# Kernel optimization log

Measured on AMD Instinct MI355X. Metric: run time of the kernel, lower is better.

Reference implementation:

```python
import jax, jax.numpy as jnp
import numpy as np

H = 256          # decoder_size
V = 3            # vocab_size
MAX_LENGTH = 64


def lstm_cell(x, h, c, Wih, Whh, b):
    # PyTorch gate order: i, f, g, o
    g = x @ Wih.T + h @ Whh.T + b
    i, f, gg, o = jnp.split(g, 4, axis=-1)
    c = jax.nn.sigmoid(f) * c + jax.nn.sigmoid(i) * jnp.tanh(gg)
    h = jax.nn.sigmoid(o) * jnp.tanh(c)
    return h, c


def setup_inputs() -> dict:
    key = jax.random.key(0)
    ks = jax.random.split(key, 16)
    T, B, F = 512, 32, 1024
    s = 1.0 / np.sqrt(H)
    u = lambda k, shape: jax.random.uniform(k, shape, jnp.float32, -s, s)
    return dict(
        cnn_feats=jax.random.normal(ks[0], (T, B, F), jnp.float32),
        # bidirectional encoder LSTM (1 layer)
        enc_Wih_f=u(ks[1], (4 * H, F)), enc_Whh_f=u(ks[2], (4 * H, H)), enc_b_f=u(ks[3], (4 * H,)),
        enc_Wih_b=u(ks[4], (4 * H, F)), enc_Whh_b=u(ks[5], (4 * H, H)), enc_b_b=u(ks[6], (4 * H,)),
        # 2-layer decoder LSTM
        dec_Wih0=u(ks[7], (4 * H, H)), dec_Whh0=u(ks[8], (4 * H, H)), dec_b0=u(ks[9], (4 * H,)),
        dec_Wih1=u(ks[10], (4 * H, H)), dec_Whh1=u(ks[11], (4 * H, H)), dec_b1=u(ks[12], (4 * H,)),
        # per-step output projection
        lin_W=u(ks[13], (V, H)), lin_b=u(ks[14], (V,)),
    )


def _forward(cnn_feats, enc_Wih_f, enc_Whh_f, enc_b_f, enc_Wih_b, enc_Whh_b, enc_b_b,
             dec_Wih0, dec_Whh0, dec_b0, dec_Wih1, dec_Whh1, dec_b1, lin_W, lin_b):
    B = cnn_feats.shape[1]
    z = jnp.zeros((B, H), cnn_feats.dtype)

    def run_dir(seq, Wih, Whh, b):
        def step(carry, x):
            h, c = lstm_cell(x, carry[0], carry[1], Wih, Whh, b)
            return (h, c), None
        (h, c), _ = jax.lax.scan(step, (z, z), seq)
        return h, c

    # encoder final states: fwd over seq, bwd over reversed seq
    hf, cf = run_dir(cnn_feats, enc_Wih_f, enc_Whh_f, enc_b_f)
    hb, cb = run_dir(cnn_feats[::-1], enc_Wih_b, enc_Whh_b, enc_b_b)

    # decoder: layer0 init = fwd-dir state, layer1 init = bwd-dir state
    def dstep(carry, _):
        x, h0, c0, h1, c1 = carry
        h0, c0 = lstm_cell(x, h0, c0, dec_Wih0, dec_Whh0, dec_b0)
        h1, c1 = lstm_cell(h0, h1, c1, dec_Wih1, dec_Whh1, dec_b1)
        y = h1 @ lin_W.T + lin_b
        return (h1, h0, c0, h1, c1), y

    _, ys = jax.lax.scan(dstep, (z, hf, cf, hb, cb), None, length=MAX_LENGTH)
    return ys  # (MAX_LENGTH, B, V)


def reference(cnn_feats, enc_Wih_f, enc_Whh_f, enc_b_f, enc_Wih_b, enc_Whh_b, enc_b_b,
              dec_Wih0, dec_Whh0, dec_b0, dec_Wih1, dec_Whh1, dec_b1, lin_W, lin_b):
    return _forward(cnn_feats, enc_Wih_f, enc_Whh_f, enc_b_f, enc_Wih_b, enc_Whh_b, enc_b_b,
                    dec_Wih0, dec_Whh0, dec_b0, dec_Wih1, dec_Whh1, dec_b1, lin_W, lin_b)
```

## Files before the change

### kernel.cpp

```cpp
#include <hip/hip_runtime.h>
#include <stdint.h>
#include <stddef.h>

typedef __attribute__((ext_vector_type(8))) short  short8;
typedef __attribute__((ext_vector_type(4))) float  floatx4;
typedef unsigned long long u64;

#define SENT 0xAAAAAAAAAAAAAAAAull

static __device__ __forceinline__ float b2f(uint16_t h) {
  union { uint32_t u; float f; } v; v.u = ((uint32_t)h) << 16; return v.f;
}
static __device__ __forceinline__ uint16_t f2b(float f) {
  union { float f; uint32_t u; } v; v.f = f;
  uint32_t u = v.u;
  uint32_t r = u + 0x7FFFu + ((u >> 16) & 1u);
  return (uint16_t)(r >> 16);
}
static __device__ __forceinline__ float sigm(float x)  { return 1.0f / (1.0f + __expf(-x)); }
static __device__ __forceinline__ float tanh_f(float x){ return 1.0f - 2.0f / (1.0f + __expf(2.0f * x)); }

static __device__ __forceinline__ floatx4 mfma16(short8 a, short8 b, floatx4 c) {
  return __builtin_amdgcn_mfma_f32_16x16x32_bf16(a, b, c, 0, 0, 0);
}
static __device__ __forceinline__ short8 cvt8(const float* p) {
  short8 r;
  #pragma unroll
  for (int i = 0; i < 8; ++i) r[i] = (short)f2b(p[i]);
  return r;
}
static __device__ __forceinline__ u64 ld_h64(const u64* p) {
  return __hip_atomic_load(p, __ATOMIC_RELAXED, __HIP_MEMORY_SCOPE_AGENT);
}
static __device__ __forceinline__ void st_h64(uint16_t* p, u64 v) {
  __hip_atomic_store((u64*)p, v, __ATOMIC_RELAXED, __HIP_MEMORY_SCOPE_AGENT);
}
static __device__ __forceinline__ void poll8(const u64* p, u64* o) {
  for (;;) {
    bool ok = true;
    #pragma unroll
    for (int i = 0; i < 8; ++i) { o[i] = ld_h64(p + i); ok &= (o[i] != SENT); }
    if (ok) break;
    __builtin_amdgcn_s_sleep(1);
  }
}

#define H 256
#define FH 1024
#define BATCH 32
#define TSEQ 512
#define DSTEPS 64
#define ERING 8

__global__ __launch_bounds__(256) void gemm_xw(
    const float* __restrict__ A, const float* __restrict__ W,
    const float* __restrict__ bias, void* __restrict__ Cout, int out_f32)
{
  const int K = 1024, N = 1024;
  __shared__ uint16_t Ah[64 * 40], Al[64 * 40];
  __shared__ uint16_t Wh[64 * 40], Wl[64 * 40];
  const int m0 = blockIdx.x * 64;
  const int n0 = blockIdx.y * 64;
  const int tid = threadIdx.x;
  const int lane = tid & 63, w = tid >> 6;
  const int wm = w & 1, wn = w >> 1;
  const int l15 = lane & 15, q4 = lane >> 4;
  const int ldrow = tid >> 2, ldk = (tid & 3) * 8;

  floatx4 acc[2][2];
  for (int i = 0; i < 2; ++i) for (int j = 0; j < 2; ++j) acc[i][j] = (floatx4){0.f,0.f,0.f,0.f};

  for (int kb = 0; kb < K; kb += 32) {
    float aa[8], ww[8];
    {
      const float4* ap = (const float4*)(A + (size_t)(m0 + ldrow) * K + kb + ldk);
      const float4* wp = (const float4*)(W + (size_t)(n0 + ldrow) * K + kb + ldk);
      *(float4*)(aa) = ap[0]; *(float4*)(aa + 4) = ap[1];
      *(float4*)(ww) = wp[0]; *(float4*)(ww + 4) = wp[1];
    }
    short8 ah, al, wh, wl;
    #pragma unroll
    for (int i = 0; i < 8; ++i) {
      uint16_t h = f2b(aa[i]); ah[i] = (short)h; al[i] = (short)f2b(aa[i] - b2f(h));
      uint16_t g = f2b(ww[i]); wl[i] = (short)f2b(ww[i] - b2f(f2b(ww[i]) ? 0 : 0));
      wh[i] = (short)f2b(ww[i]); wl[i] = (short)f2b(ww[i] - b2f((uint16_t)wh[i]));
    }
    __syncthreads();
    *(short8*)(Ah + ldrow * 40 + ldk) = ah;
    *(short8*)(Al + ldrow * 40 + ldk) = al;
    *(short8*)(Wh + ldrow * 40 + ldk) = wh;
    *(short8*)(Wl + ldrow * 40 + ldk) = wl;
    __syncthreads();
    short8 afh[2], afl[2], bfh[2], bfl[2];
    #pragma unroll
    for (int mt = 0; mt < 2; ++mt) {
      afh[mt] = *(const short8*)(Ah + (wm * 32 + mt * 16 + l15) * 40 + q4 * 8);
      afl[mt] = *(const short8*)(Al + (wm * 32 + mt * 16 + l15) * 40 + q4 * 8);
    }
    #pragma unroll
    for (int nt = 0; nt < 2; ++nt) {
      bfh[nt] = *(const short8*)(Wh + (wn * 32 + nt * 16 + l15) * 40 + q4 * 8);
      bfl[nt] = *(const short8*)(Wl + (wn * 32 + nt * 16 + l15) * 40 + q4 * 8);
    }
    #pragma unroll
    for (int mt = 0; mt < 2; ++mt)
      #pragma unroll
      for (int nt = 0; nt < 2; ++nt) {
        acc[mt][nt] = mfma16(afh[mt], bfh[nt], acc[mt][nt]);
        acc[mt][nt] = mfma16(afh[mt], bfl[nt], acc[mt][nt]);
        acc[mt][nt] = mfma16(afl[mt], bfh[nt], acc[mt][nt]);
      }
  }
  #pragma unroll
  for (int mt = 0; mt < 2; ++mt)
    #pragma unroll
    for (int nt = 0; nt < 2; ++nt) {
      const int col = n0 + wn * 32 + nt * 16 + l15;
      const float bv = bias[col];
      #pragma unroll
      for (int r = 0; r < 4; ++r) {
        const int row = m0 + wm * 32 + mt * 16 + q4 * 4 + r;
        const float v = acc[mt][nt][r] + bv;
        if (out_f32) ((float*)Cout)[(size_t)row * N + col] = v;
        else         ((uint16_t*)Cout)[(size_t)row * N + col] = f2b(v);
      }
    }
}

__global__ __launch_bounds__(256, 1) void enc_rnn(
    const void* __restrict__ XgF, const void* __restrict__ XgB, int xg_f32,
    const float* __restrict__ WhhF, const float* __restrict__ WhhB,
    uint16_t* __restrict__ hslots,
    uint16_t* __restrict__ hfin, float* __restrict__ cfin)
{
  const int d = blockIdx.x >> 3, q = blockIdx.x & 7;
  const void*  Xg  = d ? XgB : XgF;
  const float* Whh = d ? WhhB : WhhF;
  uint16_t* hsl = hslots + d * (ERING * BATCH * H);
  const int jOff = q * 32;
  const int tid = threadIdx.x, lane = tid & 63, w = tid >> 6;
  const int tt = w & 1, nt = w >> 1, l15 = lane & 15, q4 = lane >> 4;
  const int b = nt * 16 + l15;
  const int jg = jOff + tt * 16 + q4 * 4;

  __shared__ uint16_t hS[2][32 * 264];
  __shared__ float    xgS[2][32 * 132];

  short8 Af[4][8];
  #pragma unroll
  for (int g = 0; g < 4; ++g) {
    const int grow = g * H + jOff + tt * 16 + l15;
    #pragma unroll
    for (int ks = 0; ks < 8; ++ks)
      Af[g][ks] = cvt8(Whh + (size_t)grow * H + ks * 32 + q4 * 8);
  }
  for (int i = tid; i < 32 * 264; i += 256) hS[0][i] = 0;

  float cc[4] = {0.f, 0.f, 0.f, 0.f};
  union HV { uint16_t u16[4]; u64 v; } hv; hv.v = 0ull;
  const int rb = tid >> 3, seg = tid & 7;
  const int cp = seg * 16;
  const int gge = cp >> 5, jj = cp & 31;

  for (int s = 0; s < TSEQ; ++s) {
    const int t = d ? (TSEQ - 1 - s) : s;
    const int p = s & 1;
    float xv[16];
    {
      const size_t base = (size_t)(t * BATCH + rb) * FH + gge * H + jOff + jj;
      if (xg_f32) {
        const float4* xs = (const float4*)((const float*)Xg + base);
        *(float4*)(xv) = xs[0]; *(float4*)(xv + 4) = xs[1];
        *(float4*)(xv + 8) = xs[2]; *(float4*)(xv + 12) = xs[3];
      } else {
        const uint16_t* xs = (const uint16_t*)Xg + base;
        #pragma unroll
        for (int i = 0; i < 16; ++i) xv[i] = b2f(xs[i]);
      }
    }

    if (s > 0) {
      u64 tmp[8];
      const u64* ps = (const u64*)(hsl + ((s - 1) & (ERING - 1)) * (BATCH * H) + rb * H + seg * 32);
      poll8(ps, tmp);
      #pragma unroll
      for (int i = 0; i < 8; ++i)
        *(u64*)(hS[p] + rb * 264 + seg * 32 + i * 4) = tmp[i];
    }
    if (s >= 2)
      st_h64(hsl + ((s - 2) & (ERING - 1)) * (BATCH * H) + b * H + jg, SENT);
    #pragma unroll
    for (int i = 0; i < 16; ++i) xgS[p][rb * 132 + cp + i] = xv[i];
    __syncthreads();

    floatx4 a0 = {0.f,0.f,0.f,0.f}, a1 = a0, a2 = a0, a3 = a0;
    #pragma unroll
    for (int ks = 0; ks < 8; ++ks) {
      short8 bfv = *(const short8*)(hS[p] + b * 264 + ks * 32 + q4 * 8);
      a0 = mfma16(Af[0][ks], bfv, a0);
      a1 = mfma16(Af[1][ks], bfv, a1);
      a2 = mfma16(Af[2][ks], bfv, a2);
      a3 = mfma16(Af[3][ks], bfv, a3);
    }
    #pragma unroll
    for (int r = 0; r < 4; ++r) {
      const int jl = tt * 16 + q4 * 4 + r;
      const float gi = a0[r] + xgS[p][b * 132 +      jl];
      const float gf = a1[r] + xgS[p][b * 132 + 32 + jl];
      const float gc = a2[r] + xgS[p][b * 132 + 64 + jl];
      const float go = a3[r] + xgS[p][b * 132 + 96 + jl];
      const float cn2 = sigm(gf) * cc[r] + sigm(gi) * tanh_f(gc);
      cc[r] = cn2;
      hv.u16[r] = f2b(sigm(go) * tanh_f(cn2));
    }
    st_h64(hsl + (s & (ERING - 1)) * (BATCH * H) + b * H + jg, hv.v);
  }
  #pragma unroll
  for (int r = 0; r < 4; ++r) {
    hfin[d * (BATCH * H) + b * H + jg + r] = hv.u16[r];
    cfin[d * (BATCH * H) + b * H + jg + r] = cc[r];
  }
}

__global__ __launch_bounds__(256, 1) void dec_rnn(
    const float* __restrict__ Wih0, const float* __restrict__ Whh0, const float* __restrict__ bb0,
    const float* __restrict__ Wih1, const float* __restrict__ Whh1, const float* __restrict__ bb1,
    const uint16_t* __restrict__ hfin, const float* __restrict__ cfin,
    uint16_t* __restrict__ h0slots,
    uint16_t* __restrict__ h1slots,
    float*    __restrict__ h1f)
{
  const int L = blockIdx.x >> 3, q = blockIdx.x & 7;
  const float* Wih = L ? Wih1 : Wih0;
  const float* Whh = L ? Whh1 : Whh0;
  const float* bs  = L ? bb1 : bb0;
  const int jOff = q * 32;
  const int tid = threadIdx.x, lane = tid & 63, w = tid >> 6;
  const int tt = w & 1, nt = w >> 1, l15 = lane & 15, q4 = lane >> 4;
  const int b = nt * 16 + l15;
  const int jg = jOff + tt * 16 + q4 * 4;

  __shared__ uint16_t xhS[2][32 * 528];

  short8 Af[4][16];
  #pragma unroll
  for (int g = 0; g < 4; ++g) {
    const int grow = g * H + jOff + tt * 16 + l15;
    #pragma unroll
    for (int ks = 0; ks < 8; ++ks) {
      Af[g][ks]     = cvt8(Wih + (size_t)grow * H + ks * 32 + q4 * 8);
      Af[g][8 + ks] = cvt8(Whh + (size_t)grow * H + ks * 32 + q4 * 8);
    }
  }
  float brg[4][4];
  #pragma unroll
  for (int g = 0; g < 4; ++g)
    #pragma unroll
    for (int r = 0; r < 4; ++r)
      brg[g][r] = bs[g * H + jOff + tt * 16 + q4 * 4 + r];

  float cc[4];
  #pragma unroll
  for (int r = 0; r < 4; ++r) cc[r] = cfin[L * (BATCH * H) + b * H + jg + r];

  const int rb = tid >> 3, seg = tid & 7;
  const size_t off = (size_t)rb * H + seg * 32;
  union HV { uint16_t u16[4]; u64 v; } hv; hv.v = 0ull;

  for (int t = 0; t < DSTEPS; ++t) {
    const int p = t & 1;
    u64 tx[8], th[8];
    if (t == 0) {
      const u64* ph = (const u64*)(hfin + L * (BATCH * H) + off);
      #pragma unroll
      for (int i = 0; i < 8; ++i) th[i] = ph[i];
    } else {
      const uint16_t* hb = (L ? h1slots : h0slots) + (size_t)(t - 1) * (BATCH * H);
      poll8((const u64*)(hb + off), th);
    }
    if (L == 0) {
      if (t == 0) {
        #pragma unroll
        for (int i = 0; i < 8; ++i) tx[i] = 0ull;
      } else {
        poll8((const u64*)(h1slots + (size_t)(t - 1) * (BATCH * H) + off), tx);
      }
    } else {
      poll8((const u64*)(h0slots + (size_t)t * (BATCH * H) + off), tx);
    }
    #pragma unroll
    for (int i = 0; i < 8; ++i) {
      *(u64*)(xhS[p] + rb * 528 + seg * 32 + i * 4) = tx[i];
      *(u64*)(xhS[p] + rb * 528 + 256 + seg * 32 + i * 4) = th[i];
    }
    __syncthreads();

    floatx4 a0 = {0.f,0.f,0.f,0.f}, a1 = a0, a2 = a0, a3 = a0;
    #pragma unroll
    for (int ks = 0; ks < 16; ++ks) {
      short8 bfv = *(const short8*)(xhS[p] + b * 528 + ks * 32 + q4 * 8);
      a0 = mfma16(Af[0][ks], bfv, a0);
      a1 = mfma16(Af[1][ks], bfv, a1);
      a2 = mfma16(Af[2][ks], bfv, a2);
      a3 = mfma16(Af[3][ks], bfv, a3);
    }
    float hval[4];
    #pragma unroll
    for (int r = 0; r < 4; ++r) {
      const float gi = a0[r] + brg[0][r];
      const float gf = a1[r] + brg[1][r];
      const float gc = a2[r] + brg[2][r];
      const float go = a3[r] + brg[3][r];
      const float cn2 = sigm(gf) * cc[r] + sigm(gi) * tanh_f(gc);
      cc[r] = cn2;
      hval[r] = sigm(go) * tanh_f(cn2);
      hv.u16[r] = f2b(hval[r]);
    }
    st_h64((L ? h1slots : h0slots) + (size_t)t * (BATCH * H) + b * H + jg, hv.v);
    if (L == 1) {
      float* df = h1f + (size_t)t * (BATCH * H) + b * H + jg;
      #pragma unroll
      for (int r = 0; r < 4; ++r) df[r] = hval[r];
    }
  }
}

__global__ __launch_bounds__(256) void out_proj(
    const float* __restrict__ h1f, const float* __restrict__ linW,
    const float* __restrict__ linb, float* __restrict__ out)
{
  const int idx = blockIdx.x * 256 + threadIdx.x;
  if (idx >= DSTEPS * BATCH * 3) return;
  const int v = idx % 3;
  const int tb = idx / 3;
  const float* hrow = h1f + (size_t)tb * H;
  const float* wrow = linW + (size_t)v * H;
  float s = linb[v];
  for (int k = 0; k < H; ++k) s += hrow[k] * wrow[k];
  out[idx] = s;
}

extern "C" void kernel_launch(void* const* d_in, const int* in_sizes, int n_in,
                              void* d_out, int out_size, void* d_ws, size_t ws_size,
                              hipStream_t stream) {
  (void)in_sizes; (void)n_in; (void)out_size;
  const float* cnn   = (const float*)d_in[0];
  const float* WihF  = (const float*)d_in[1];
  const float* WhhF  = (const float*)d_in[2];
  const float* bF    = (const float*)d_in[3];
  const float* WihB  = (const float*)d_in[4];
  const float* WhhB  = (const float*)d_in[5];
  const float* bB    = (const float*)d_in[6];
  const float* Wih0  = (const float*)d_in[7];
  const float* Whh0  = (const float*)d_in[8];
  const float* b0    = (const float*)d_in[9];
  const float* Wih1  = (const float*)d_in[10];
  const float* Whh1  = (const float*)d_in[11];
  const float* b1    = (const float*)d_in[12];
  const float* linW  = (const float*)d_in[13];
  const float* linb  = (const float*)d_in[14];

  const size_t XG_ELEMS = (size_t)TSEQ * BATCH * FH;
  const size_t SMALL = 2457600;
  const int xg_f32 = (ws_size >= 2 * XG_ELEMS * 4 + SMALL) ? 1 : 0;
  const size_t S = XG_ELEMS * (xg_f32 ? 4 : 2);

  uint8_t* ws = (uint8_t*)d_ws;
  void*     XgF    = (void*)(ws);
  void*     XgB    = (void*)(ws + S);
  float*    h1f    = (float*)(ws + S);
  uint8_t*  base   = ws + 2 * S;
  uint16_t* hslotsE = (uint16_t*)(base);
  uint16_t* h0slots = (uint16_t*)(base + 262144);
  uint16_t* h1slots = (uint16_t*)(base + 1310720);
  uint16_t* hfin    = (uint16_t*)(base + 2359296);
  float*    cfin    = (float*)(base + 2392064);

  hipMemsetAsync(base, 0xAA, 2359296, stream);

  gemm_xw<<<dim3(256, 16), 256, 0, stream>>>(cnn, WihF, bF, XgF, xg_f32);
  gemm_xw<<<dim3(256, 16), 256, 0, stream>>>(cnn, WihB, bB, XgB, xg_f32);
  enc_rnn<<<16, 256, 0, stream>>>(XgF, XgB, xg_f32, WhhF, WhhB,
                                  hslotsE, hfin, cfin);
  dec_rnn<<<16, 256, 0, stream>>>(Wih0, Whh0, b0, Wih1, Whh1, b1,
                                  hfin, cfin, h0slots, h1slots, h1f);
  out_proj<<<24, 256, 0, stream>>>(h1f, linW, linb, (float*)d_out);
}
```

Baseline: 2.587 ms.

## Poll hidden-state fragments directly into MFMA registers, dropping LDS staging and barriers

The encoder and decoder recurrent kernels no longer stage polled hidden states and input gates through shared memory behind __syncthreads. Each lane now polls exactly the MFMA B-fragment it needs with cache-bypassing dwordx4 inline-asm loads and feeds it straight to the MFMAs. The encoder also prefetches the next step's input-gate values into registers and resets the ring slot from further back, which widens the slack before a slot is reused. Each lane now reads redundant global data, and correctness relies on slot-reset ordering across a deeper ring lag and a periodic atomic-load fallback in the poll loop.

```diff
diff --git a/kernel.cpp b/kernel.cpp
--- a/kernel.cpp
+++ b/kernel.cpp
@@ -4,6 +4,7 @@
 
 typedef __attribute__((ext_vector_type(8))) short  short8;
 typedef __attribute__((ext_vector_type(4))) float  floatx4;
+typedef __attribute__((ext_vector_type(4))) unsigned int u32x4;
 typedef unsigned long long u64;
 
 #define SENT 0xAAAAAAAAAAAAAAAAull
@@ -29,17 +30,90 @@
   for (int i = 0; i < 8; ++i) r[i] = (short)f2b(p[i]);
   return r;
 }
+
+static __device__ __forceinline__ void st_h64(uint16_t* p, u64 v) {
+  __hip_atomic_store((u64*)p, v, __ATOMIC_RELAXED, __HIP_MEMORY_SCOPE_AGENT);
+}
 static __device__ __forceinline__ u64 ld_h64(const u64* p) {
   return __hip_atomic_load(p, __ATOMIC_RELAXED, __HIP_MEMORY_SCOPE_AGENT);
 }
-static __device__ __forceinline__ void st_h64(uint16_t* p, u64 v) {
-  __hip_atomic_store((u64*)p, v, __ATOMIC_RELAXED, __HIP_MEMORY_SCOPE_AGENT);
-}
-static __device__ __forceinline__ void poll8(const u64* p, u64* o) {
+static __device__ __forceinline__ bool frag_ok(u32x4 v) {
+  const u64 lo = ((u64)v[1] << 32) | v[0];
+  const u64 hi = ((u64)v[3] << 32) | v[2];
+  return (lo != SENT) & (hi != SENT);
+}
+static __device__ __forceinline__ void ld8x16(const uint16_t* p, u32x4* o) {
+  asm volatile(
+      "global_load_dwordx4 %0, %8, off sc0 sc1\n\t"
+      "global_load_dwordx4 %1, %8, off offset:64 sc0 sc1\n\t"
+      "global_load_dwordx4 %2, %8, off offset:128 sc0 sc1\n\t"
+      "global_load_dwordx4 %3, %8, off offset:192 sc0 sc1\n\t"
+      "global_load_dwordx4 %4, %8, off offset:256 sc0 sc1\n\t"
+      "global_load_dwordx4 %5, %8, off offset:320 sc0 sc1\n\t"
+      "global_load_dwordx4 %6, %8, off offset:384 sc0 sc1\n\t"
+      "global_load_dwordx4 %7, %8, off offset:448 sc0 sc1\n\t"
+      "s_waitcnt vmcnt(0)"
+      : "=&v"(o[0]), "=&v"(o[1]), "=&v"(o[2]), "=&v"(o[3]),
+        "=&v"(o[4]), "=&v"(o[5]), "=&v"(o[6]), "=&v"(o[7])
+      : "v"(p)
+      : "memory");
+}
+static __device__ __forceinline__ void ld16x16(const uint16_t* pa, const uint16_t* pb,
+                                               u32x4* oa, u32x4* ob) {
+  asm volatile(
+      "global_load_dwordx4 %0, %16, off sc0 sc1\n\t"
+      "global_load_dwordx4 %1, %16, off offset:64 sc0 sc1\n\t"
+      "global_load_dwordx4 %2, %16, off offset:128 sc0 sc1\n\t"
+      "global_load_dwordx4 %3, %16, off offset:192 sc0 sc1\n\t"
+      "global_load_dwordx4 %4, %16, off offset:256 sc0 sc1\n\t"
+      "global_load_dwordx4 %5, %16, off offset:320 sc0 sc1\n\t"
+      "global_load_dwordx4 %6, %16, off offset:384 sc0 sc1\n\t"
+      "global_load_dwordx4 %7, %16, off offset:448 sc0 sc1\n\t"
+      "global_load_dwordx4 %8, %17, off sc0 sc1\n\t"
+      "global_load_dwordx4 %9, %17, off offset:64 sc0 sc1\n\t"
+      "global_load_dwordx4 %10, %17, off offset:128 sc0 sc1\n\t"
+      "global_load_dwordx4 %11, %17, off offset:192 sc0 sc1\n\t"
+      "global_load_dwordx4 %12, %17, off offset:256 sc0 sc1\n\t"
+      "global_load_dwordx4 %13, %17, off offset:320 sc0 sc1\n\t"
+      "global_load_dwordx4 %14, %17, off offset:384 sc0 sc1\n\t"
+      "global_load_dwordx4 %15, %17, off offset:448 sc0 sc1\n\t"
+      "s_waitcnt vmcnt(0)"
+      : "=&v"(oa[0]), "=&v"(oa[1]), "=&v"(oa[2]), "=&v"(oa[3]),
+        "=&v"(oa[4]), "=&v"(oa[5]), "=&v"(oa[6]), "=&v"(oa[7]),
+        "=&v"(ob[0]), "=&v"(ob[1]), "=&v"(ob[2]), "=&v"(ob[3]),
+        "=&v"(ob[4]), "=&v"(ob[5]), "=&v"(ob[6]), "=&v"(ob[7])
+      : "v"(pa), "v"(pb)
+      : "memory");
+}
+static __device__ __forceinline__ void valve8(const uint16_t* p, u32x4* o) {
+  const u64* q = (const u64*)p;
+  #pragma unroll
+  for (int k = 0; k < 8; ++k) {
+    u64 a = ld_h64(q + k * 8), c = ld_h64(q + k * 8 + 1);
+    o[k][0] = (unsigned)a; o[k][1] = (unsigned)(a >> 32);
+    o[k][2] = (unsigned)c; o[k][3] = (unsigned)(c >> 32);
+  }
+}
+static __device__ __forceinline__ void poll8f(const uint16_t* p, u32x4* o) {
+  int it = 0;
   for (;;) {
+    if ((++it & 1023) == 0) valve8(p, o); else ld8x16(p, o);
     bool ok = true;
     #pragma unroll
-    for (int i = 0; i < 8; ++i) { o[i] = ld_h64(p + i); ok &= (o[i] != SENT); }
+    for (int k = 0; k < 8; ++k) ok &= frag_ok(o[k]);
+    if (ok) break;
+    __builtin_amdgcn_s_sleep(1);
+  }
+}
+static __device__ __forceinline__ void poll16f(const uint16_t* pa, const uint16_t* pb,
+                                               u32x4* oa, u32x4* ob) {
+  int it = 0;
+  for (;;) {
+    if ((++it & 1023) == 0) { valve8(pa, oa); valve8(pb, ob); }
+    else ld16x16(pa, pb, oa, ob);
+    bool ok = true;
+    #pragma unroll
+    for (int k = 0; k < 8; ++k) ok &= frag_ok(oa[k]) & frag_ok(ob[k]);
     if (ok) break;
     __builtin_amdgcn_s_sleep(1);
   }
@@ -82,8 +156,7 @@
     #pragma unroll
     for (int i = 0; i < 8; ++i) {
       uint16_t h = f2b(aa[i]); ah[i] = (short)h; al[i] = (short)f2b(aa[i] - b2f(h));
-      uint16_t g = f2b(ww[i]); wl[i] = (short)f2b(ww[i] - b2f(f2b(ww[i]) ? 0 : 0));
-      wh[i] = (short)f2b(ww[i]); wl[i] = (short)f2b(ww[i] - b2f((uint16_t)wh[i]));
+      uint16_t g = f2b(ww[i]); wh[i] = (short)g; wl[i] = (short)f2b(ww[i] - b2f(g));
     }
     __syncthreads();
     *(short8*)(Ah + ldrow * 40 + ldk) = ah;
@@ -143,9 +216,6 @@
   const int b = nt * 16 + l15;
   const int jg = jOff + tt * 16 + q4 * 4;
 
-  __shared__ uint16_t hS[2][32 * 264];
-  __shared__ float    xgS[2][32 * 132];
-
   short8 Af[4][8];
   #pragma unroll
   for (int g = 0; g < 4; ++g) {
@@ -154,66 +224,64 @@
     for (int ks = 0; ks < 8; ++ks)
       Af[g][ks] = cvt8(Whh + (size_t)grow * H + ks * 32 + q4 * 8);
   }
-  for (int i = tid; i < 32 * 264; i += 256) hS[0][i] = 0;
 
   float cc[4] = {0.f, 0.f, 0.f, 0.f};
   union HV { uint16_t u16[4]; u64 v; } hv; hv.v = 0ull;
-  const int rb = tid >> 3, seg = tid & 7;
-  const int cp = seg * 16;
-  const int gge = cp >> 5, jj = cp & 31;
+
+  float xvf[16];
+  u64   xvb[4];
+  auto ldx = [&](int s2) {
+    const int t2 = d ? (TSEQ - 1 - s2) : s2;
+    const size_t bas = (size_t)(t2 * BATCH + b) * FH + jg;
+    if (xg_f32) {
+      const float* xp = (const float*)Xg + bas;
+      *(float4*)(xvf + 0)  = *(const float4*)(xp);
+      *(float4*)(xvf + 4)  = *(const float4*)(xp + H);
+      *(float4*)(xvf + 8)  = *(const float4*)(xp + 2 * H);
+      *(float4*)(xvf + 12) = *(const float4*)(xp + 3 * H);
+    } else {
+      const uint16_t* xp = (const uint16_t*)Xg + bas;
+      xvb[0] = *(const u64*)(xp);
+      xvb[1] = *(const u64*)(xp + H);
+      xvb[2] = *(const u64*)(xp + 2 * H);
+      xvb[3] = *(const u64*)(xp + 3 * H);
+    }
+  };
+  ldx(0);
 
   for (int s = 0; s < TSEQ; ++s) {
-    const int t = d ? (TSEQ - 1 - s) : s;
-    const int p = s & 1;
-    float xv[16];
-    {
-      const size_t base = (size_t)(t * BATCH + rb) * FH + gge * H + jOff + jj;
-      if (xg_f32) {
-        const float4* xs = (const float4*)((const float*)Xg + base);
-        *(float4*)(xv) = xs[0]; *(float4*)(xv + 4) = xs[1];
-        *(float4*)(xv + 8) = xs[2]; *(float4*)(xv + 12) = xs[3];
-      } else {
-        const uint16_t* xs = (const uint16_t*)Xg + base;
-        #pragma unroll
-        for (int i = 0; i < 16; ++i) xv[i] = b2f(xs[i]);
+    floatx4 a0 = {0.f,0.f,0.f,0.f}, a1 = a0, a2 = a0, a3 = a0;
+    if (s > 0) {
+      u32x4 pol[8];
+      const uint16_t* ps = hsl + ((s - 1) & (ERING - 1)) * (BATCH * H) + b * H + q4 * 8;
+      poll8f(ps, pol);
+      #pragma unroll
+      for (int ks = 0; ks < 8; ++ks) {
+        short8 bfv = *(short8*)&pol[ks];
+        a0 = mfma16(Af[0][ks], bfv, a0);
+        a1 = mfma16(Af[1][ks], bfv, a1);
+        a2 = mfma16(Af[2][ks], bfv, a2);
+        a3 = mfma16(Af[3][ks], bfv, a3);
       }
     }
-
-    if (s > 0) {
-      u64 tmp[8];
-      const u64* ps = (const u64*)(hsl + ((s - 1) & (ERING - 1)) * (BATCH * H) + rb * H + seg * 32);
-      poll8(ps, tmp);
-      #pragma unroll
-      for (int i = 0; i < 8; ++i)
-        *(u64*)(hS[p] + rb * 264 + seg * 32 + i * 4) = tmp[i];
-    }
-    if (s >= 2)
-      st_h64(hsl + ((s - 2) & (ERING - 1)) * (BATCH * H) + b * H + jg, SENT);
-    #pragma unroll
-    for (int i = 0; i < 16; ++i) xgS[p][rb * 132 + cp + i] = xv[i];
-    __syncthreads();
-
-    floatx4 a0 = {0.f,0.f,0.f,0.f}, a1 = a0, a2 = a0, a3 = a0;
-    #pragma unroll
-    for (int ks = 0; ks < 8; ++ks) {
-      short8 bfv = *(const short8*)(hS[p] + b * 264 + ks * 32 + q4 * 8);
-      a0 = mfma16(Af[0][ks], bfv, a0);
-      a1 = mfma16(Af[1][ks], bfv, a1);
-      a2 = mfma16(Af[2][ks], bfv, a2);
-      a3 = mfma16(Af[3][ks], bfv, a3);
-    }
     #pragma unroll
     for (int r = 0; r < 4; ++r) {
-      const int jl = tt * 16 + q4 * 4 + r;
-      const float gi = a0[r] + xgS[p][b * 132 +      jl];
-      const float gf = a1[r] + xgS[p][b * 132 + 32 + jl];
-      const float gc = a2[r] + xgS[p][b * 132 + 64 + jl];
-      const float go = a3[r] + xgS[p][b * 132 + 96 + jl];
+      const float x0 = xg_f32 ? xvf[0 + r]  : b2f((uint16_t)(xvb[0] >> (16 * r)));
+      const float x1 = xg_f32 ? xvf[4 + r]  : b2f((uint16_t)(xvb[1] >> (16 * r)));
+      const float x2 = xg_f32 ? xvf[8 + r]  : b2f((uint16_t)(xvb[2] >> (16 * r)));
+      const float x3 = xg_f32 ? xvf[12 + r] : b2f((uint16_t)(xvb[3] >> (16 * r)));
+      const float gi = a0[r] + x0;
+      const float gf = a1[r] + x1;
+      const float gc = a2[r] + x2;
+      const float go = a3[r] + x3;
       const float cn2 = sigm(gf) * cc[r] + sigm(gi) * tanh_f(gc);
       cc[r] = cn2;
       hv.u16[r] = f2b(sigm(go) * tanh_f(cn2));
     }
     st_h64(hsl + (s & (ERING - 1)) * (BATCH * H) + b * H + jg, hv.v);
+    if (s >= 6)
+      st_h64(hsl + ((s - 6) & (ERING - 1)) * (BATCH * H) + b * H + jg, SENT);
+    if (s + 1 < TSEQ) ldx(s + 1);
   }
   #pragma unroll
   for (int r = 0; r < 4; ++r) {
@@ -240,8 +308,6 @@
   const int b = nt * 16 + l15;
   const int jg = jOff + tt * 16 + q4 * 4;
 
-  __shared__ uint16_t xhS[2][32 * 528];
-
   short8 Af[4][16];
   #pragma unroll
   for (int g = 0; g < 4; ++g) {
@@ -263,42 +329,34 @@
   #pragma unroll
   for (int r = 0; r < 4; ++r) cc[r] = cfin[L * (BATCH * H) + b * H + jg + r];
 
-  const int rb = tid >> 3, seg = tid & 7;
-  const size_t off = (size_t)rb * H + seg * 32;
+  uint16_t*       hOwn = L ? h1slots : h0slots;
+  const uint16_t* hX   = L ? h0slots : h1slots;
+  const int fo = b * H + q4 * 8;
   union HV { uint16_t u16[4]; u64 v; } hv; hv.v = 0ull;
 
   for (int t = 0; t < DSTEPS; ++t) {
-    const int p = t & 1;
-    u64 tx[8], th[8];
+    u32x4 pol[16];
     if (t == 0) {
-      const u64* ph = (const u64*)(hfin + L * (BATCH * H) + off);
+      const uint16_t* ph = hfin + L * (BATCH * H) + fo;
       #pragma unroll
-      for (int i = 0; i < 8; ++i) th[i] = ph[i];
-    } else {
-      const uint16_t* hb = (L ? h1slots : h0slots) + (size_t)(t - 1) * (BATCH * H);
-      poll8((const u64*)(hb + off), th);
-    }
-    if (L == 0) {
-      if (t == 0) {
+      for (int k = 0; k < 8; ++k) pol[8 + k] = *(const u32x4*)(ph + k * 32);
+      if (L == 0) {
         #pragma unroll
-        for (int i = 0; i < 8; ++i) tx[i] = 0ull;
+        for (int k = 0; k < 8; ++k) pol[k] = (u32x4){0u, 0u, 0u, 0u};
       } else {
-        poll8((const u64*)(h1slots + (size_t)(t - 1) * (BATCH * H) + off), tx);
+        poll8f(hX + fo, pol);
       }
     } else {
-      poll8((const u64*)(h0slots + (size_t)t * (BATCH * H) + off), tx);
-    }
-    #pragma unroll
-    for (int i = 0; i < 8; ++i) {
-      *(u64*)(xhS[p] + rb * 528 + seg * 32 + i * 4) = tx[i];
-      *(u64*)(xhS[p] + rb * 528 + 256 + seg * 32 + i * 4) = th[i];
-    }
-    __syncthreads();
+      const uint16_t* pOwn = hOwn + (size_t)(t - 1) * (BATCH * H) + fo;
+      const uint16_t* pX   = L ? (hX + (size_t)t * (BATCH * H) + fo)
+                               : (hX + (size_t)(t - 1) * (BATCH * H) + fo);
+      poll16f(pX, pOwn, pol, pol + 8);
+    }
 
     floatx4 a0 = {0.f,0.f,0.f,0.f}, a1 = a0, a2 = a0, a3 = a0;
     #pragma unroll
     for (int ks = 0; ks < 16; ++ks) {
-      short8 bfv = *(const short8*)(xhS[p] + b * 528 + ks * 32 + q4 * 8);
+      short8 bfv = *(short8*)&pol[ks];
       a0 = mfma16(Af[0][ks], bfv, a0);
       a1 = mfma16(Af[1][ks], bfv, a1);
       a2 = mfma16(Af[2][ks], bfv, a2);
@@ -316,7 +374,7 @@
       hval[r] = sigm(go) * tanh_f(cn2);
       hv.u16[r] = f2b(hval[r]);
     }
-    st_h64((L ? h1slots : h0slots) + (size_t)t * (BATCH * H) + b * H + jg, hv.v);
+    st_h64(hOwn + (size_t)t * (BATCH * H) + b * H + jg, hv.v);
     if (L == 1) {
       float* df = h1f + (size_t)t * (BATCH * H) + b * H + jg;
       #pragma unroll
```

Result: faster. 2.471 ms (-4.5%).
